# Kernel tuning notes

Measured on AMD Instinct MI355X. Metric: run time of the kernel, lower is better.

## Reference

```python
import jax, jax.numpy as jnp
import numpy as np

B, S, D_MODEL = 64, 2048, 512
NUM_UNITS = 512
WINDOW = 128  # attention_window_size


def setup_inputs() -> dict:
    key = jax.random.key(0)
    k1, k2, k3, k4, k5 = jax.random.split(key, 5)
    query = jax.random.normal(k1, (B, D_MODEL), dtype=jnp.float32)
    keys = jax.random.normal(k2, (B, S, D_MODEL), dtype=jnp.float32)
    key_lengths = jax.random.randint(k3, (B,), 0, 256, dtype=jnp.int32)
    Wq = jax.random.normal(k4, (NUM_UNITS, D_MODEL), dtype=jnp.float32) * 0.04
    wp = jax.random.normal(k5, (1, NUM_UNITS), dtype=jnp.float32) * 0.04
    return {"query": query, "keys": keys, "key_lengths": key_lengths, "Wq": Wq, "wp": wp}


def reference(query, keys, key_lengths, Wq, wp):
    # dot score: [B, S]
    score = jnp.einsum('bd,bsd->bs', query, keys)
    weight = jax.nn.softmax(score, axis=-1)

    # predictive local alignment
    L = key_lengths.astype(jnp.float32)[:, None]                      # [B, 1]
    activated = jnp.tanh(query @ Wq.T)                                # [B, num_units]
    sig = jax.nn.sigmoid(activated @ wp.T)                            # [B, 1]
    p = L * sig                                                       # [B, 1] predicted alignment point

    # window bounds via .int() truncation toward zero
    start = jnp.trunc(p - WINDOW).astype(jnp.int32)                   # [B, 1]
    end = jnp.trunc(p + WINDOW).astype(jnp.int32)                     # [B, 1]

    # gaussian factor (note: original uses L - p, a per-row scalar; 2*std = WINDOW)
    g = jnp.exp(-((L - p) ** 2) / WINDOW)                             # [B, 1]
    weight = weight * g                                               # [B, S]

    # per-row dynamic window gather + weighted sum, done as masked reduction
    pos = jnp.arange(S, dtype=jnp.int32)[None, :]                     # [1, S]
    mask = (pos >= start) & (pos < end)                               # [B, S]
    w = jnp.where(mask, weight, jnp.zeros((), dtype=weight.dtype))
    total_context = jnp.einsum('bs,bsd->bd', w, keys)                 # [B, d]
    return total_context, score
```

## Files before the change

### kernel.cpp

```cpp
#include <hip/hip_runtime.h>
#include <math.h>

#define BB 64
#define SS 2048
#define DD 512
#define NU 512
#define WIN 128
#define NSLICE 4
#define PART_OFF 1024

__device__ __forceinline__ float wave_reduce_sum(float v) {
    #pragma unroll
    for (int off = 32; off > 0; off >>= 1)
        v += __shfl_down(v, off, 64);
    return v;
}

__device__ __forceinline__ float wave_reduce_max(float v) {
    #pragma unroll
    for (int off = 32; off > 0; off >>= 1)
        v = fmaxf(v, __shfl_down(v, off, 64));
    return v;
}

__device__ __forceinline__ float dot4(const float4 a, const float4 b) {
    return a.x * b.x + a.y * b.y + a.z * b.z + a.w * b.w;
}

__global__ __launch_bounds__(256, 4) void score_p_kernel(const float* __restrict__ query,
                                                         const float* __restrict__ keys,
                                                         const int* __restrict__ key_lengths,
                                                         const float* __restrict__ Wq,
                                                         const float* __restrict__ wp,
                                                         float* __restrict__ score,
                                                         float* __restrict__ ws) {
    const int t    = threadIdx.x;
    const int wave = t >> 6;
    const int lane = t & 63;
    const int g    = lane >> 4;
    const int w    = lane & 15;

    if (blockIdx.x < BB) {
        const int b = blockIdx.x;
        __shared__ float act[NU];
        __shared__ float wsum[4];

        const float4* qv = (const float4*)(query + b * DD);
        const float4 q0 = qv[w],       q1 = qv[16 + w],  q2 = qv[32 + w],  q3 = qv[48 + w];
        const float4 q4 = qv[64 + w],  q5 = qv[80 + w],  q6 = qv[96 + w],  q7 = qv[112 + w];

        #pragma unroll 2
        for (int pass = 0; pass < 32; ++pass) {
            const int u = pass * 16 + wave * 4 + g;
            const float4* rv = (const float4*)(Wq + (size_t)u * DD);
            const float4 k0 = rv[w],       k1 = rv[16 + w],  k2 = rv[32 + w],  k3 = rv[48 + w];
            const float4 k4 = rv[64 + w],  k5 = rv[80 + w],  k6 = rv[96 + w],  k7 = rv[112 + w];
            const float s0 = dot4(k0, q0), s1 = dot4(k1, q1), s2 = dot4(k2, q2), s3 = dot4(k3, q3);
            const float s4 = dot4(k4, q4), s5 = dot4(k5, q5), s6 = dot4(k6, q6), s7 = dot4(k7, q7);
            float acc = ((s0 + s1) + (s2 + s3)) + ((s4 + s5) + (s6 + s7));
            #pragma unroll
            for (int m = 1; m < 16; m <<= 1)
                acc += __shfl_xor(acc, m, 64);
            if (w == 0) act[u] = tanhf(acc);
        }
        __syncthreads();

        float sv = act[t] * wp[t] + act[t + 256] * wp[t + 256];
        sv = wave_reduce_sum(sv);
        if (lane == 0) wsum[wave] = sv;
        __syncthreads();

        if (t == 0) {
            const float s = wsum[0] + wsum[1] + wsum[2] + wsum[3];
            const float sig = 1.0f / (1.0f + expf(-s));
            const float L = (float)key_lengths[b];
            const float p = L * sig;
            const int start = (int)(p - (float)WIN);
            const int end   = (int)(p + (float)WIN);
            const float diff = L - p;
            const float gg = expf(-(diff * diff) / (float)WIN);
            ws[b] = gg;
            ((int*)ws)[BB + b]     = start;
            ((int*)ws)[2 * BB + b] = end;
        }
    } else {
        const int bid   = blockIdx.x - BB;
        const int b     = bid >> 5;
        const int chunk = bid & 31;
        const int r0    = chunk * 64 + wave * 16;

        const float4* qv = (const float4*)(query + b * DD);
        const float4 q0 = qv[w],       q1 = qv[16 + w],  q2 = qv[32 + w],  q3 = qv[48 + w];
        const float4 q4 = qv[64 + w],  q5 = qv[80 + w],  q6 = qv[96 + w],  q7 = qv[112 + w];

        const float4* kb = (const float4*)(keys + (size_t)b * SS * DD);

        const float4* rv = kb + (size_t)(r0 + g) * (DD / 4);
        float4 k0 = rv[w],       k1 = rv[16 + w],  k2 = rv[32 + w],  k3 = rv[48 + w];
        float4 k4 = rv[64 + w],  k5 = rv[80 + w],  k6 = rv[96 + w],  k7 = rv[112 + w];

        #pragma unroll
        for (int p = 0; p < 4; ++p) {
            float4 n0, n1, n2, n3, n4, n5, n6, n7;
            if (p < 3) {
                const float4* nv = kb + (size_t)(r0 + (p + 1) * 4 + g) * (DD / 4);
                n0 = nv[w];       n1 = nv[16 + w];  n2 = nv[32 + w];  n3 = nv[48 + w];
                n4 = nv[64 + w];  n5 = nv[80 + w];  n6 = nv[96 + w];  n7 = nv[112 + w];
            }
            const float s0 = dot4(k0, q0), s1 = dot4(k1, q1), s2 = dot4(k2, q2), s3 = dot4(k3, q3);
            const float s4 = dot4(k4, q4), s5 = dot4(k5, q5), s6 = dot4(k6, q6), s7 = dot4(k7, q7);
            float acc = ((s0 + s1) + (s2 + s3)) + ((s4 + s5) + (s6 + s7));
            #pragma unroll
            for (int m = 1; m < 16; m <<= 1)
                acc += __shfl_xor(acc, m, 64);
            if (w == 0) score[b * SS + r0 + p * 4 + g] = acc;
            if (p < 3) {
                k0 = n0; k1 = n1; k2 = n2; k3 = n3;
                k4 = n4; k5 = n5; k6 = n6; k7 = n7;
            }
        }
    }
}

__global__ __launch_bounds__(256) void ctxA_kernel(const float* __restrict__ keys,
                                                   const float* __restrict__ score,
                                                   const float* __restrict__ ws,
                                                   float* __restrict__ part) {
    const int b     = blockIdx.x;
    const int slice = blockIdx.y;
    const int t     = threadIdx.x;
    const int wave  = t >> 6;
    const int lane  = t & 63;

    __shared__ float w_lds[80];
    __shared__ float redm[4], reds[4];
    __shared__ float4 part_l[128];

    const float* srow = score + b * SS;

    const float4 v0 = ((const float4*)srow)[t];
    const float4 v1 = ((const float4*)srow)[t + 256];
    float m = fmaxf(fmaxf(fmaxf(v0.x, v0.y), fmaxf(v0.z, v0.w)),
                    fmaxf(fmaxf(v1.x, v1.y), fmaxf(v1.z, v1.w)));
    m = wave_reduce_max(m);
    if (lane == 0) redm[wave] = m;
    __syncthreads();
    const float mx = fmaxf(fmaxf(redm[0], redm[1]), fmaxf(redm[2], redm[3]));

    float sum = expf(v0.x - mx) + expf(v0.y - mx) + expf(v0.z - mx) + expf(v0.w - mx)
              + expf(v1.x - mx) + expf(v1.y - mx) + expf(v1.z - mx) + expf(v1.w - mx);
    sum = wave_reduce_sum(sum);
    if (lane == 0) reds[wave] = sum;
    __syncthreads();
    const float inv = 1.0f / (reds[0] + reds[1] + reds[2] + reds[3]);

    const float gg   = ws[b];
    const int start  = ((const int*)ws)[BB + b];
    const int end    = ((const int*)ws)[2 * BB + b];
    const int s_lo   = max(start, 0);
    const int s_hi   = min(end, SS);
    const int width  = s_hi - s_lo;
    const int sliceN = (width + NSLICE - 1) / NSLICE;
    const int i_lo   = slice * sliceN;
    const int i_hi   = min(i_lo + sliceN, width);
    const int n      = i_hi - i_lo;

    for (int i = t; i < n; i += 256)
        w_lds[i] = expf(srow[s_lo + i_lo + i] - mx) * inv * gg;
    __syncthreads();

    const int myrow = t >> 7;
    const int c4    = t & 127;
    const float4* kb = (const float4*)(keys + ((size_t)b * SS + s_lo + i_lo) * DD);

    float4 acc = make_float4(0.f, 0.f, 0.f, 0.f);
    for (int i = myrow; i < n; i += 2) {
        const float4 k = kb[(size_t)i * (DD / 4) + c4];
        const float wg = w_lds[i];
        acc.x += wg * k.x; acc.y += wg * k.y; acc.z += wg * k.z; acc.w += wg * k.w;
    }

    if (myrow) part_l[c4] = acc;
    __syncthreads();
    if (!myrow) {
        const float4 o = part_l[c4];
        acc.x += o.x; acc.y += o.y; acc.z += o.z; acc.w += o.w;
        ((float4*)part)[((size_t)b * NSLICE + slice) * 128 + c4] = acc;
    }
}

__global__ __launch_bounds__(512) void ctxB_kernel(const float* __restrict__ part,
                                                   float* __restrict__ ctx) {
    const int b = blockIdx.x;
    const int d = threadIdx.x;
    float s = 0.f;
    #pragma unroll
    for (int sl = 0; sl < NSLICE; ++sl)
        s += part[((size_t)b * NSLICE + sl) * DD + d];
    ctx[b * DD + d] = s;
}

extern "C" void kernel_launch(void* const* d_in, const int* in_sizes, int n_in,
                              void* d_out, int out_size, void* d_ws, size_t ws_size,
                              hipStream_t stream) {
    const float* query       = (const float*)d_in[0];
    const float* keys        = (const float*)d_in[1];
    const int*   key_lengths = (const int*)d_in[2];
    const float* Wq          = (const float*)d_in[3];
    const float* wp          = (const float*)d_in[4];

    float* ctx   = (float*)d_out;
    float* score = (float*)d_out + BB * DD;
    float* ws    = (float*)d_ws;
    float* part  = (float*)d_ws + PART_OFF;

    hipLaunchKernelGGL(score_p_kernel, dim3(BB + BB * 32), dim3(256), 0, stream,
                       query, keys, key_lengths, Wq, wp, score, ws);
    hipLaunchKernelGGL(ctxA_kernel, dim3(BB, NSLICE), dim3(256), 0, stream,
                       keys, score, ws, part);
    hipLaunchKernelGGL(ctxB_kernel, dim3(BB), dim3(512), 0, stream,
                       part, ctx);
}
```

Baseline: 67.39 us.

## Fuse final slice reduction into ctxA via atomic counter; double score blocks and slices

Removes the separate ctxB kernel launch. ctxA now increments a per-batch atomic counter, and the last slice block to finish sums the partial results into ctx. The score kernel uses twice as many blocks with half the rows each, and the context gather splits into 8 slices instead of 4. The intent is lower launch overhead and more parallelism, at the cost of atomics, threadfences and more redundant softmax recomputation, since each slice still reads the whole score row.

Result: slower. 81.23 us (+20.5%).

```diff
diff --git a/kernel.cpp b/kernel.cpp
--- a/kernel.cpp
+++ b/kernel.cpp
@@ -6,7 +6,11 @@
 #define DD 512
 #define NU 512
 #define WIN 128
-#define NSLICE 4
+#define NSLICE 8
+#define G_OFF   0
+#define ST_OFF  64
+#define EN_OFF  128
+#define CNT_OFF 192
 #define PART_OFF 1024
 
 __device__ __forceinline__ float wave_reduce_sum(float v) {
@@ -44,6 +48,8 @@
         const int b = blockIdx.x;
         __shared__ float act[NU];
         __shared__ float wsum[4];
+
+        if (t == 0) ((int*)ws)[CNT_OFF + b] = 0;
 
         const float4* qv = (const float4*)(query + b * DD);
         const float4 q0 = qv[w],       q1 = qv[16 + w],  q2 = qv[32 + w],  q3 = qv[48 + w];
@@ -79,15 +85,15 @@
             const int end   = (int)(p + (float)WIN);
             const float diff = L - p;
             const float gg = expf(-(diff * diff) / (float)WIN);
-            ws[b] = gg;
-            ((int*)ws)[BB + b]     = start;
-            ((int*)ws)[2 * BB + b] = end;
+            ws[G_OFF + b] = gg;
+            ((int*)ws)[ST_OFF + b] = start;
+            ((int*)ws)[EN_OFF + b] = end;
         }
     } else {
         const int bid   = blockIdx.x - BB;
-        const int b     = bid >> 5;
-        const int chunk = bid & 31;
-        const int r0    = chunk * 64 + wave * 16;
+        const int b     = bid >> 6;
+        const int chunk = bid & 63;
+        const int r0    = chunk * 32 + wave * 8;
 
         const float4* qv = (const float4*)(query + b * DD);
         const float4 q0 = qv[w],       q1 = qv[16 + w],  q2 = qv[32 + w],  q3 = qv[48 + w];
@@ -100,10 +106,10 @@
         float4 k4 = rv[64 + w],  k5 = rv[80 + w],  k6 = rv[96 + w],  k7 = rv[112 + w];
 
         #pragma unroll
-        for (int p = 0; p < 4; ++p) {
+        for (int p = 0; p < 2; ++p) {
             float4 n0, n1, n2, n3, n4, n5, n6, n7;
-            if (p < 3) {
-                const float4* nv = kb + (size_t)(r0 + (p + 1) * 4 + g) * (DD / 4);
+            if (p < 1) {
+                const float4* nv = kb + (size_t)(r0 + 4 + g) * (DD / 4);
                 n0 = nv[w];       n1 = nv[16 + w];  n2 = nv[32 + w];  n3 = nv[48 + w];
                 n4 = nv[64 + w];  n5 = nv[80 + w];  n6 = nv[96 + w];  n7 = nv[112 + w];
             }
@@ -114,7 +120,7 @@
             for (int m = 1; m < 16; m <<= 1)
                 acc += __shfl_xor(acc, m, 64);
             if (w == 0) score[b * SS + r0 + p * 4 + g] = acc;
-            if (p < 3) {
+            if (p < 1) {
                 k0 = n0; k1 = n1; k2 = n2; k3 = n3;
                 k4 = n4; k5 = n5; k6 = n6; k7 = n7;
             }
@@ -124,17 +130,19 @@
 
 __global__ __launch_bounds__(256) void ctxA_kernel(const float* __restrict__ keys,
                                                    const float* __restrict__ score,
-                                                   const float* __restrict__ ws,
-                                                   float* __restrict__ part) {
+                                                   float* __restrict__ ws,
+                                                   float* __restrict__ part,
+                                                   float* __restrict__ ctx) {
     const int b     = blockIdx.x;
     const int slice = blockIdx.y;
     const int t     = threadIdx.x;
     const int wave  = t >> 6;
     const int lane  = t & 63;
 
-    __shared__ float w_lds[80];
+    __shared__ float w_lds[40];
     __shared__ float redm[4], reds[4];
     __shared__ float4 part_l[128];
+    __shared__ int is_last;
 
     const float* srow = score + b * SS;
 
@@ -154,9 +162,9 @@
     __syncthreads();
     const float inv = 1.0f / (reds[0] + reds[1] + reds[2] + reds[3]);
 
-    const float gg   = ws[b];
-    const int start  = ((const int*)ws)[BB + b];
-    const int end    = ((const int*)ws)[2 * BB + b];
+    const float gg   = ws[G_OFF + b];
+    const int start  = ((const int*)ws)[ST_OFF + b];
+    const int end    = ((const int*)ws)[EN_OFF + b];
     const int s_lo   = max(start, 0);
     const int s_hi   = min(end, SS);
     const int width  = s_hi - s_lo;
@@ -187,17 +195,27 @@
         acc.x += o.x; acc.y += o.y; acc.z += o.z; acc.w += o.w;
         ((float4*)part)[((size_t)b * NSLICE + slice) * 128 + c4] = acc;
     }
-}
-
-__global__ __launch_bounds__(512) void ctxB_kernel(const float* __restrict__ part,
-                                                   float* __restrict__ ctx) {
-    const int b = blockIdx.x;
-    const int d = threadIdx.x;
-    float s = 0.f;
-    #pragma unroll
-    for (int sl = 0; sl < NSLICE; ++sl)
-        s += part[((size_t)b * NSLICE + sl) * DD + d];
-    ctx[b * DD + d] = s;
+    __syncthreads();
+
+    if (t == 0) {
+        __threadfence();
+        const int old = atomicAdd((int*)ws + CNT_OFF + b, 1);
+        is_last = (old == NSLICE - 1);
+    }
+    __syncthreads();
+
+    if (is_last) {
+        __threadfence();
+        #pragma unroll
+        for (int rep = 0; rep < 2; ++rep) {
+            const int d = t + rep * 256;
+            float s = 0.f;
+            #pragma unroll
+            for (int sl = 0; sl < NSLICE; ++sl)
+                s += part[((size_t)b * NSLICE + sl) * DD + d];
+            ctx[b * DD + d] = s;
+        }
+    }
 }
 
 extern "C" void kernel_launch(void* const* d_in, const int* in_sizes, int n_in,
@@ -214,10 +232,8 @@
     float* ws    = (float*)d_ws;
     float* part  = (float*)d_ws + PART_OFF;
 
-    hipLaunchKernelGGL(score_p_kernel, dim3(BB + BB * 32), dim3(256), 0, stream,
+    hipLaunchKernelGGL(score_p_kernel, dim3(BB + BB * 64), dim3(256), 0, stream,
                        query, keys, key_lengths, Wq, wp, score, ws);
     hipLaunchKernelGGL(ctxA_kernel, dim3(BB, NSLICE), dim3(256), 0, stream,
-                       keys, score, ws, part);
-    hipLaunchKernelGGL(ctxB_kernel, dim3(BB), dim3(512), 0, stream,
-                       part, ctx);
-}
+                       keys, score, ws, part, ctx);
+}
```
